# Optimization experiments

Hardware: AMD Instinct MI355X
Metric: run time of the kernel (lower is better)

## Reference

```python
import jax, jax.numpy as jnp
from jax import lax
import numpy as np

# ---- SLAYER SRM-alpha neuron / simulation constants (net_params) ----
THETA = 10.0      # spiking threshold
TAU_SR = 1.0      # PSP (synaptic response) time constant
TAU_REF = 1.0     # refractory time constant
TS = 1.0          # simulation timestep
POOL_GAIN = 1.1 * THETA  # SLAYER pool layer uses fixed weights = 1.1*theta (sum pool)

# SRM alpha kernel eps[n] = (n*Ts/tau) * exp(1 - n*Ts/tau) = c * n * d^n with
#   d = exp(-Ts/tau), c = e*Ts/tau.  Causal convolution with this kernel obeys
# a 2nd-order linear recurrence, so we implement psp as a lax.scan over time
# (the "recursive exponential temporal filter" the original does via temporal conv).

def psp(x):
    """Alpha-kernel temporal filter along last (time) axis."""
    d = float(np.exp(-TS / TAU_SR))
    c = float(np.e * TS / TAU_SR)
    xt = jnp.moveaxis(x, -1, 0)  # (T, ...)
    z = jnp.zeros_like(xt[0])
    def step(carry, u):
        p, q = carry
        q = d * (q + p)       # q[t] = sum_{n>=1} n d^n x[t-n]
        p = d * p + u         # p[t] = sum_{n>=0} d^n x[t-n]
        return (p, q), c * q
    _, y = lax.scan(step, (z, z), xt)
    return jnp.moveaxis(y, 0, -1)


def spike(u):
    """SLAYER spike generation: threshold the membrane potential at theta and
    subtract a refractory alpha kernel (-2*theta * alpha(tauRef)) from the
    future potential after each spike. Sequential scan over time."""
    d = float(np.exp(-TS / TAU_REF))
    c_r = float(-2.0 * THETA * np.e * TS / TAU_REF)
    ut = jnp.moveaxis(u, -1, 0)  # (T, ...)
    z = jnp.zeros_like(ut[0])
    def step(carry, u_t):
        p, q = carry
        q = d * (q + p)                       # refractory filter state
        s = (u_t + c_r * q >= THETA).astype(u_t.dtype)
        p = d * p + s                         # spikes feed the refractory filter
        return (p, q), s
    _, s = lax.scan(step, (z, z), ut)
    return jnp.moveaxis(s, 0, -1) / TS


def pool(x, k):
    """SLAYER pool: conv with fixed weight 1.1*theta (sum pool scaled)."""
    B, C, H, W, T = x.shape
    xr = x.reshape(B, C, H // k, k, W // k, k, T)
    return POOL_GAIN * xr.sum(axis=(3, 5))


def conv2d_t(x, W, pad):
    """Per-timestep 2D conv (SLAYER conv has time-kernel 1, no bias)."""
    B, C, H, Wd, T = x.shape
    xf = jnp.moveaxis(x, -1, 1).reshape(B * T, C, H, Wd)
    y = lax.conv_general_dilated(xf, W, (1, 1), [(pad, pad), (pad, pad)],
                                 dimension_numbers=('NCHW', 'OIHW', 'NCHW'))
    O, Ho, Wo = y.shape[1], y.shape[2], y.shape[3]
    return jnp.moveaxis(y.reshape(B, T, O, Ho, Wo), 1, -1)


def setup_inputs() -> dict:
    key = jax.random.key(0)
    ks = jax.random.split(key, 5)
    B, T = 8, 300
    s_in = jax.random.bernoulli(ks[0], 0.1, (B, 2, 128, 128, T)).astype(jnp.float32)
    # weightScale 10/50/... only affects init magnitude; choose scales that
    # produce non-degenerate spiking activity.
    W1 = jax.random.normal(ks[1], (16, 2, 5, 5), jnp.float32) * 0.5
    W2 = jax.random.normal(ks[2], (32, 16, 3, 3), jnp.float32) * 0.2
    Wf1 = jax.random.normal(ks[3], (512, 32, 8, 8), jnp.float32) * 0.05
    Wf2 = jax.random.normal(ks[4], (11, 512), jnp.float32) * 0.2
    return {"s_in": s_in, "W1": W1, "W2": W2, "Wf1": Wf1, "Wf2": Wf2}


def reference(s_in, W1, W2, Wf1, Wf2):
    s = spike(psp(pool(s_in, 4)))                 # SP0: (B,2,32,32,T)
    s = spike(psp(conv2d_t(s, W1, 2)))            # SC1: (B,16,32,32,T)
    s = spike(psp(pool(s, 2)))                    # SP1: (B,16,16,16,T)
    # SDC dropout p=0.0 -> identity
    s = spike(psp(conv2d_t(s, W2, 1)))            # SC2: (B,32,16,16,T)
    s = spike(psp(pool(s, 2)))                    # SP2: (B,32,8,8,T)
    # SDF dropout p=0.0 -> identity
    s = spike(psp(jnp.einsum('bchwt,ochw->bot', s, Wf1)))  # SF1: (B,512,T)
    s = spike(psp(jnp.einsum('bct,oc->bot', s, Wf2)))      # SF2: (B,11,T)
    return s
```

## Files before the change

### kernel.cpp

```cpp
#include <hip/hip_runtime.h>
#include <stdint.h>

#define T_STEPS 300
#define T4 75

__device__ __forceinline__ void scan_step(float x, float& pp, float& pq,
                                          float& rp, float& rq, float& s_out) {
    const float D  = 0.36787944117144233f;
    const float C  = 2.7182818284590452f;
    const float CR = -54.365636569180904f;
    const float TH = 10.0f;
    pq = D * (pq + pp);
    pp = D * pp + x;
    float u = C * pq;
    rq = D * (rq + rp);
    float s = (u + CR * rq >= TH) ? 1.0f : 0.0f;
    rp = D * rp + s;
    s_out = s;
}

#define SCAN4(v, PACK)                                                     \
    {                                                                      \
        float s0, s1, s2, s3;                                              \
        scan_step(v.x, pp, pq, rp, rq, s0);                                \
        scan_step(v.y, pp, pq, rp, rq, s1);                                \
        scan_step(v.z, pp, pq, rp, rq, s2);                                \
        scan_step(v.w, pp, pq, rp, rq, s3);                                \
        PACK = (uint32_t)s0 | ((uint32_t)s1 << 8) |                        \
               ((uint32_t)s2 << 16) | ((uint32_t)s3 << 24);                \
    }

#define FMA4(A, wc) A.x = fmaf(wc, f0, A.x); A.y = fmaf(wc, f1, A.y); \
                    A.z = fmaf(wc, f2, A.z); A.w = fmaf(wc, f3, A.w);

__global__ __launch_bounds__(256) void k_pool4(const float* __restrict__ in,
                                               float* __restrict__ z) {
    int idx = blockIdx.x * 256 + threadIdx.x;
    int t4 = idx % T4;
    int n  = idx / T4;
    int x = n & 31, y = (n >> 5) & 31, bc = n >> 10;
    const float* base = in + ((size_t)bc * 16384 + (size_t)(4 * y) * 128 + 4 * x) * T_STEPS + 4 * t4;
    float4 acc = {0.f, 0.f, 0.f, 0.f};
#pragma unroll
    for (int i = 0; i < 4; ++i)
#pragma unroll
        for (int j = 0; j < 4; ++j) {
            float4 v = *reinterpret_cast<const float4*>(base + ((size_t)i * 128 + j) * T_STEPS);
            acc.x += v.x; acc.y += v.y; acc.z += v.z; acc.w += v.w;
        }
    float4 o = {11.f * acc.x, 11.f * acc.y, 11.f * acc.z, 11.f * acc.w};
    *reinterpret_cast<float4*>(z + (size_t)n * T_STEPS + 4 * t4) = o;
}

__global__ __launch_bounds__(256) void k_scan_l0(const float* __restrict__ z,
                                                 uint32_t* __restrict__ sp, int N) {
    int n = blockIdx.x * 256 + threadIdx.x;
    if (n >= N) return;
    const float4* zp = reinterpret_cast<const float4*>(z + (size_t)n * T_STEPS);
    float pp = 0.f, pq = 0.f, rp = 0.f, rq = 0.f;
#pragma unroll 2
    for (int t4 = 0; t4 < T4; ++t4) {
        float4 v = zp[t4];
        uint32_t pack;
        SCAN4(v, pack);
        sp[(size_t)t4 * N + n] = pack;
    }
}

__global__ __launch_bounds__(256) void k_scan_plane(const float4* __restrict__ z,
                                                    uint32_t* __restrict__ sp, int N) {
    int n = blockIdx.x * 256 + threadIdx.x;
    if (n >= N) return;
    float pp = 0.f, pq = 0.f, rp = 0.f, rq = 0.f;
#pragma unroll 2
    for (int t4 = 0; t4 < T4; ++t4) {
        float4 v = z[(size_t)t4 * N + n];
        uint32_t pack;
        SCAN4(v, pack);
        sp[(size_t)t4 * N + n] = pack;
    }
}

__global__ __launch_bounds__(256) void k_scan_f32(const float* __restrict__ z,
                                                  float* __restrict__ s, int N, int ostride) {
    int n = blockIdx.x * blockDim.x + threadIdx.x;
    if (n >= N) return;
    const float4* zp = reinterpret_cast<const float4*>(z + (size_t)n * T_STEPS);
    float* spo = s + (size_t)n * ostride;
    float pp = 0.f, pq = 0.f, rp = 0.f, rq = 0.f;
    for (int it = 0; it < T4; ++it) {
        float4 v = zp[it];
        float4 o;
        scan_step(v.x, pp, pq, rp, rq, o.x);
        scan_step(v.y, pp, pq, rp, rq, o.y);
        scan_step(v.z, pp, pq, rp, rq, o.z);
        scan_step(v.w, pp, pq, rp, rq, o.w);
        *reinterpret_cast<float4*>(spo + it * 4) = o;
    }
}

template<int HW, int NIN, int NOUT>
__global__ __launch_bounds__(256) void k_pool2s(const uint32_t* __restrict__ sin,
                                                uint32_t* __restrict__ sout) {
    int n = blockIdx.x * 256 + threadIdx.x;
    if (n >= NOUT) return;
    int x = n % HW, y = (n / HW) % HW, bc = n / (HW * HW);
    const int W2d = HW * 2;
    const uint32_t* base0 = sin + (size_t)bc * W2d * W2d + (size_t)(2 * y) * W2d + 2 * x;
    float pp = 0.f, pq = 0.f, rp = 0.f, rq = 0.f;
#pragma unroll 2
    for (int t4 = 0; t4 < T4; ++t4) {
        const uint32_t* p = base0 + (size_t)t4 * NIN;
        uint32_t sum = p[0] + p[1] + p[W2d] + p[W2d + 1];
        float4 v;
        v.x = 11.f * (float)(sum & 0xffu);
        v.y = 11.f * (float)((sum >> 8) & 0xffu);
        v.z = 11.f * (float)((sum >> 16) & 0xffu);
        v.w = 11.f * (float)(sum >> 24);
        uint32_t pack;
        SCAN4(v, pack);
        sout[(size_t)t4 * NOUT + n] = pack;
    }
}

__global__ __launch_bounds__(256) void k_conv1(const uint32_t* __restrict__ s0p,
                                               const float* __restrict__ W1,
                                               float4* __restrict__ z1p) {
    __shared__ float w_lds[2][25][16];
    int bid = blockIdx.x;
    int pixblk = bid & 3;
    int t4 = (bid >> 2) % 75;
    int b  = bid / 300;
    int tid = threadIdx.x;
    for (int j = tid; j < 800; j += 256) {
        int o = j & 15, kk = (j >> 4) % 25, c = j / 400;
        w_lds[c][kk][o] = W1[(o * 2 + c) * 25 + kk];
    }
    __syncthreads();
    int pix = pixblk * 256 + tid;
    int px = pix & 31, py = pix >> 5;
    float4 acc[16];
#pragma unroll
    for (int o = 0; o < 16; ++o) acc[o] = make_float4(0.f, 0.f, 0.f, 0.f);
    const uint32_t* pb = s0p + (size_t)t4 * 16384 + (size_t)(b * 2) * 1024;
    for (int c = 0; c < 2; ++c) {
#pragma unroll
        for (int ky = 0; ky < 5; ++ky) {
            int yy = py + ky - 2;
            bool rok = (unsigned)yy < 32u;
#pragma unroll
            for (int kx = 0; kx < 5; ++kx) {
                int xx = px + kx - 2;
                uint32_t v = 0;
                if (rok && (unsigned)xx < 32u) v = pb[c * 1024 + yy * 32 + xx];
                float f0 = (float)(v & 0xffu), f1 = (float)((v >> 8) & 0xffu);
                float f2 = (float)((v >> 16) & 0xffu), f3 = (float)(v >> 24);
                int kk = ky * 5 + kx;
#pragma unroll
                for (int oo = 0; oo < 4; ++oo) {
                    float4 w4 = *reinterpret_cast<const float4*>(&w_lds[c][kk][oo * 4]);
                    FMA4(acc[oo * 4 + 0], w4.x);
                    FMA4(acc[oo * 4 + 1], w4.y);
                    FMA4(acc[oo * 4 + 2], w4.z);
                    FMA4(acc[oo * 4 + 3], w4.w);
                }
            }
        }
    }
    size_t zb = (size_t)t4 * 131072 + (size_t)(b * 16) * 1024 + pix;
#pragma unroll
    for (int o = 0; o < 16; ++o) z1p[zb + o * 1024] = acc[o];
}

__global__ __launch_bounds__(256) void k_conv2(const uint32_t* __restrict__ s2p,
                                               const float* __restrict__ W2,
                                               float4* __restrict__ z2p) {
    __shared__ float w_lds[16][9][16];
    int bid = blockIdx.x;
    int oh = bid & 1;
    int t4 = (bid >> 1) % 75;
    int b  = bid / 150;
    int tid = threadIdx.x;
    for (int j = tid; j < 2304; j += 256) {
        int o = j & 15;
        int t9 = (j >> 4) % 9;
        int c  = j / 144;
        w_lds[c][t9][o] = W2[(size_t)((oh * 16 + o) * 16 + c) * 9 + t9];
    }
    __syncthreads();
    int px = tid & 15, py = tid >> 4;
    float4 acc[16];
#pragma unroll
    for (int o = 0; o < 16; ++o) acc[o] = make_float4(0.f, 0.f, 0.f, 0.f);
    const uint32_t* pb = s2p + (size_t)t4 * 32768 + (size_t)(b * 16) * 256;
    for (int c = 0; c < 16; ++c) {
#pragma unroll
        for (int ky = 0; ky < 3; ++ky) {
            int yy = py + ky - 1;
            bool rok = (unsigned)yy < 16u;
#pragma unroll
            for (int kx = 0; kx < 3; ++kx) {
                int xx = px + kx - 1;
                uint32_t v = 0;
                if (rok && (unsigned)xx < 16u) v = pb[c * 256 + yy * 16 + xx];
                float f0 = (float)(v & 0xffu), f1 = (float)((v >> 8) & 0xffu);
                float f2 = (float)((v >> 16) & 0xffu), f3 = (float)(v >> 24);
                int t9 = ky * 3 + kx;
#pragma unroll
                for (int oo = 0; oo < 4; ++oo) {
                    float4 w4 = *reinterpret_cast<const float4*>(&w_lds[c][t9][oo * 4]);
                    FMA4(acc[oo * 4 + 0], w4.x);
                    FMA4(acc[oo * 4 + 1], w4.y);
                    FMA4(acc[oo * 4 + 2], w4.z);
                    FMA4(acc[oo * 4 + 3], w4.w);
                }
            }
        }
    }
    size_t zb = (size_t)t4 * 65536 + (size_t)(b * 32 + oh * 16) * 256 + tid;
#pragma unroll
    for (int o = 0; o < 16; ++o) z2p[zb + o * 256] = acc[o];
}

__global__ __launch_bounds__(256) void k_fc1_gemm(const uint32_t* __restrict__ s4p,
                                                  const float* __restrict__ Wf1,
                                                  float* __restrict__ z) {
    __shared__ float Wt[32][128];
    __shared__ float At[32][32];

    int tt = blockIdx.x;
    int ot = blockIdx.y;
    int b  = blockIdx.z;
    int tid = threadIdx.x;
    int othr = tid >> 3, tthr = tid & 7;
    int o0 = othr * 4;
    int t4g = tt * 8 + tthr;

    int wo = tid >> 1, wh = tid & 1;
    const float* wrow = Wf1 + (size_t)(ot * 128 + wo) * 2048 + wh * 16;
    int akk = tid & 31, at4 = tid >> 5;
    int at4g = tt * 8 + at4;
    bool aok = at4g < T4;
    const uint32_t* abase = s4p + (size_t)(aok ? at4g : 0) * 16384 + b * 2048 + akk;

    float4 acc0 = {0,0,0,0}, acc1 = {0,0,0,0}, acc2 = {0,0,0,0}, acc3 = {0,0,0,0};

    float4 wr0 = *reinterpret_cast<const float4*>(wrow + 0);
    float4 wr1 = *reinterpret_cast<const float4*>(wrow + 4);
    float4 wr2 = *reinterpret_cast<const float4*>(wrow + 8);
    float4 wr3 = *reinterpret_cast<const float4*>(wrow + 12);
    uint32_t av = aok ? abase[0] : 0u;

    for (int ks = 0; ks < 64; ++ks) {
        __syncthreads();
        int kb = wh * 16;
        Wt[kb + 0][wo] = wr0.x;  Wt[kb + 1][wo] = wr0.y;  Wt[kb + 2][wo] = wr0.z;  Wt[kb + 3][wo] = wr0.w;
        Wt[kb + 4][wo] = wr1.x;  Wt[kb + 5][wo] = wr1.y;  Wt[kb + 6][wo] = wr1.z;  Wt[kb + 7][wo] = wr1.w;
        Wt[kb + 8][wo] = wr2.x;  Wt[kb + 9][wo] = wr2.y;  Wt[kb +10][wo] = wr2.z;  Wt[kb +11][wo] = wr2.w;
        Wt[kb +12][wo] = wr3.x;  Wt[kb +13][wo] = wr3.y;  Wt[kb +14][wo] = wr3.z;  Wt[kb +15][wo] = wr3.w;
        float4 af;
        af.x = (float)(av & 0xffu);  af.y = (float)((av >> 8) & 0xffu);
        af.z = (float)((av >> 16) & 0xffu);  af.w = (float)(av >> 24);
        *reinterpret_cast<float4*>(&At[akk][at4 * 4]) = af;
        __syncthreads();
        if (ks < 63) {
            int k0 = (ks + 1) * 32;
            wr0 = *reinterpret_cast<const float4*>(wrow + k0 + 0);
            wr1 = *reinterpret_cast<const float4*>(wrow + k0 + 4);
            wr2 = *reinterpret_cast<const float4*>(wrow + k0 + 8);
            wr3 = *reinterpret_cast<const float4*>(wrow + k0 + 12);
            av = aok ? abase[k0] : 0u;
        }
#pragma unroll
        for (int kk = 0; kk < 32; ++kk) {
            float4 wv = *reinterpret_cast<const float4*>(&Wt[kk][o0]);
            float4 avv = *reinterpret_cast<const float4*>(&At[kk][tthr * 4]);
            acc0.x = fmaf(wv.x, avv.x, acc0.x); acc0.y = fmaf(wv.x, avv.y, acc0.y);
            acc0.z = fmaf(wv.x, avv.z, acc0.z); acc0.w = fmaf(wv.x, avv.w, acc0.w);
            acc1.x = fmaf(wv.y, avv.x, acc1.x); acc1.y = fmaf(wv.y, avv.y, acc1.y);
            acc1.z = fmaf(wv.y, avv.z, acc1.z); acc1.w = fmaf(wv.y, avv.w, acc1.w);
            acc2.x = fmaf(wv.z, avv.x, acc2.x); acc2.y = fmaf(wv.z, avv.y, acc2.y);
            acc2.z = fmaf(wv.z, avv.z, acc2.z); acc2.w = fmaf(wv.z, avv.w, acc2.w);
            acc3.x = fmaf(wv.w, avv.x, acc3.x); acc3.y = fmaf(wv.w, avv.y, acc3.y);
            acc3.z = fmaf(wv.w, avv.z, acc3.z); acc3.w = fmaf(wv.w, avv.w, acc3.w);
        }
    }

    if (t4g < T4) {
        size_t orow = (size_t)(b * 512 + ot * 128 + o0);
        *reinterpret_cast<float4*>(z + (orow + 0) * T_STEPS + t4g * 4) = acc0;
        *reinterpret_cast<float4*>(z + (orow + 1) * T_STEPS + t4g * 4) = acc1;
        *reinterpret_cast<float4*>(z + (orow + 2) * T_STEPS + t4g * 4) = acc2;
        *reinterpret_cast<float4*>(z + (orow + 3) * T_STEPS + t4g * 4) = acc3;
    }
}

__global__ __launch_bounds__(256) void k_fc2(const float* __restrict__ s5,
                                             const float* __restrict__ Wf2,
                                             float* __restrict__ z) {
    int idx = blockIdx.x * 256 + threadIdx.x;
    if (idx >= 6600) return;
    int t4 = idx % T4;
    int r  = idx / T4;
    int b = r & 7, o = r >> 3;
    const float* sp = s5 + (size_t)b * 512 * T_STEPS + 4 * t4;
    const float* wp = Wf2 + (size_t)o * 512;
    float a0 = 0.f, a1 = 0.f, a2 = 0.f, a3 = 0.f;
#pragma unroll 2
    for (int k = 0; k < 512; k += 4) {
        float4 wv = *reinterpret_cast<const float4*>(wp + k);
        float4 v0 = *reinterpret_cast<const float4*>(sp + (size_t)(k + 0) * T_STEPS);
        float4 v1 = *reinterpret_cast<const float4*>(sp + (size_t)(k + 1) * T_STEPS);
        float4 v2 = *reinterpret_cast<const float4*>(sp + (size_t)(k + 2) * T_STEPS);
        float4 v3 = *reinterpret_cast<const float4*>(sp + (size_t)(k + 3) * T_STEPS);
        a0 = fmaf(wv.x, v0.x, a0); a1 = fmaf(wv.x, v0.y, a1); a2 = fmaf(wv.x, v0.z, a2); a3 = fmaf(wv.x, v0.w, a3);
        a0 = fmaf(wv.y, v1.x, a0); a1 = fmaf(wv.y, v1.y, a1); a2 = fmaf(wv.y, v1.z, a2); a3 = fmaf(wv.y, v1.w, a3);
        a0 = fmaf(wv.z, v2.x, a0); a1 = fmaf(wv.z, v2.y, a1); a2 = fmaf(wv.z, v2.z, a2); a3 = fmaf(wv.z, v2.w, a3);
        a0 = fmaf(wv.w, v3.x, a0); a1 = fmaf(wv.w, v3.y, a1); a2 = fmaf(wv.w, v3.z, a2); a3 = fmaf(wv.w, v3.w, a3);
    }
    *reinterpret_cast<float4*>(z + (size_t)(b * 11 + o) * T_STEPS + 4 * t4) = make_float4(a0, a1, a2, a3);
}

__global__ void k_zero(float* out, int n) {
    int i = blockIdx.x * 256 + threadIdx.x;
    if (i < n) out[i] = 0.f;
}

extern "C" void kernel_launch(void* const* d_in, const int* in_sizes, int n_in,
                              void* d_out, int out_size, void* d_ws, size_t ws_size,
                              hipStream_t stream) {
    const float* s_in = (const float*)d_in[0];
    const float* W1   = (const float*)d_in[1];
    const float* W2   = (const float*)d_in[2];
    const float* Wf1  = (const float*)d_in[3];
    const float* Wf2  = (const float*)d_in[4];
    float* out = (float*)d_out;

    const size_t OFF_Z  = 0;
    const size_t OFF_S0 = 157286400;
    const size_t OFF_S1 = 162201600;
    const size_t OFF_S2 = 201523200;
    const size_t OFF_S3 = 211353600;
    const size_t OFF_S4 = 231014400;
    const size_t OFF_S5 = 235929600;
    const size_t NEEDED = 240844800;

    if (ws_size < NEEDED) {
        k_zero<<<(26400 + 255) / 256, 256, 0, stream>>>(out, 26400);
        return;
    }

    char* ws = (char*)d_ws;
    float*    Z   = (float*)(ws + OFF_Z);
    uint32_t* s0p = (uint32_t*)(ws + OFF_S0);
    uint32_t* s1p = (uint32_t*)(ws + OFF_S1);
    uint32_t* s2p = (uint32_t*)(ws + OFF_S2);
    uint32_t* s3p = (uint32_t*)(ws + OFF_S3);
    uint32_t* s4p = (uint32_t*)(ws + OFF_S4);
    float*    s5  = (float*)(ws + OFF_S5);

    k_pool4<<<4800, 256, 0, stream>>>(s_in, Z);
    k_scan_l0<<<64, 256, 0, stream>>>(Z, s0p, 16384);

    k_conv1<<<2400, 256, 0, stream>>>(s0p, W1, (float4*)Z);
    k_scan_plane<<<512, 256, 0, stream>>>((const float4*)Z, s1p, 131072);

    k_pool2s<16, 131072, 32768><<<128, 256, 0, stream>>>(s1p, s2p);

    k_conv2<<<1200, 256, 0, stream>>>(s2p, W2, (float4*)Z);
    k_scan_plane<<<256, 256, 0, stream>>>((const float4*)Z, s3p, 65536);

    k_pool2s<8, 65536, 16384><<<64, 256, 0, stream>>>(s3p, s4p);

    k_fc1_gemm<<<dim3(10, 4, 8), 256, 0, stream>>>(s4p, Wf1, Z);
    k_scan_f32<<<16, 256, 0, stream>>>(Z, s5, 4096, 300);

    k_fc2<<<26, 256, 0, stream>>>(s5, Wf2, Z);
    k_scan_f32<<<1, 128, 0, stream>>>(Z, out, 88, 300);
}
```

Before: 965.8 us.

## Move FC1 to bf16 MFMA with three-way split weights for fp32 accuracy

Replaces the LDS-tiled fp32 FMA GEMM for the first fully connected layer with bf16 MFMA instructions. The weights are split into high, mid and low bf16 parts on every call so the sum of three MFMAs approximates fp32 precision, and the binary spikes are exact in bf16. The pool2 spike kernel now writes bf16 spikes in a k-contiguous per-timestep layout that the MFMA operands read directly. In exchange it adds a weight-split kernel on each call, triples the weight traffic, and reads operands straight from global memory with no LDS reuse.

```diff
diff --git a/kernel.cpp b/kernel.cpp
--- a/kernel.cpp
+++ b/kernel.cpp
@@ -3,6 +3,9 @@
 
 #define T_STEPS 300
 #define T4 75
+
+typedef __attribute__((ext_vector_type(8))) short bf16x8;
+typedef __attribute__((ext_vector_type(4))) float f32x4;
 
 __device__ __forceinline__ void scan_step(float x, float& pp, float& pq,
                                           float& rp, float& rq, float& s_out) {
@@ -123,6 +126,35 @@
     }
 }
 
+__global__ __launch_bounds__(256) void k_pool2s_bf(const uint32_t* __restrict__ sin,
+                                                   ushort* __restrict__ sb) {
+    int n = blockIdx.x * 256 + threadIdx.x;
+    if (n >= 16384) return;
+    int x = n & 7, y = (n >> 3) & 7, bc = n >> 6;
+    const uint32_t* base0 = sin + (size_t)bc * 256 + (size_t)(2 * y) * 16 + 2 * x;
+    int b = n >> 11, k = n & 2047;
+    ushort* out = sb + (size_t)b * 320 * 2048 + k;
+    float pp = 0.f, pq = 0.f, rp = 0.f, rq = 0.f;
+    for (int t4 = 0; t4 < T4; ++t4) {
+        const uint32_t* p = base0 + (size_t)t4 * 65536;
+        uint32_t sum = p[0] + p[1] + p[16] + p[17];
+        float4 v;
+        v.x = 11.f * (float)(sum & 0xffu);
+        v.y = 11.f * (float)((sum >> 8) & 0xffu);
+        v.z = 11.f * (float)((sum >> 16) & 0xffu);
+        v.w = 11.f * (float)(sum >> 24);
+        float s0, s1, s2, s3;
+        scan_step(v.x, pp, pq, rp, rq, s0);
+        scan_step(v.y, pp, pq, rp, rq, s1);
+        scan_step(v.z, pp, pq, rp, rq, s2);
+        scan_step(v.w, pp, pq, rp, rq, s3);
+        out[(size_t)(t4 * 4 + 0) * 2048] = s0 != 0.f ? 0x3F80 : 0;
+        out[(size_t)(t4 * 4 + 1) * 2048] = s1 != 0.f ? 0x3F80 : 0;
+        out[(size_t)(t4 * 4 + 2) * 2048] = s2 != 0.f ? 0x3F80 : 0;
+        out[(size_t)(t4 * 4 + 3) * 2048] = s3 != 0.f ? 0x3F80 : 0;
+    }
+}
+
 __global__ __launch_bounds__(256) void k_conv1(const uint32_t* __restrict__ s0p,
                                                const float* __restrict__ W1,
                                                float4* __restrict__ z1p) {
@@ -222,76 +254,77 @@
     for (int o = 0; o < 16; ++o) z2p[zb + o * 256] = acc[o];
 }
 
-__global__ __launch_bounds__(256) void k_fc1_gemm(const uint32_t* __restrict__ s4p,
-                                                  const float* __restrict__ Wf1,
+__device__ __forceinline__ ushort f2bf(float f) {
+    uint32_t u = __float_as_uint(f);
+    u = u + 0x7fffu + ((u >> 16) & 1u);
+    return (ushort)(u >> 16);
+}
+__device__ __forceinline__ float bf2f(ushort h) {
+    return __uint_as_float((uint32_t)h << 16);
+}
+__global__ __launch_bounds__(256) void k_wsplit(const float* __restrict__ W,
+                                                ushort* __restrict__ Wh,
+                                                ushort* __restrict__ Wm,
+                                                ushort* __restrict__ Wl, int n) {
+    int i = blockIdx.x * 256 + threadIdx.x;
+    if (i >= n) return;
+    float w = W[i];
+    ushort h = f2bf(w);
+    float r1 = w - bf2f(h);
+    ushort m = f2bf(r1);
+    float r2 = r1 - bf2f(m);
+    ushort l = f2bf(r2);
+    Wh[i] = h; Wm[i] = m; Wl[i] = l;
+}
+
+__device__ __forceinline__ bf16x8 ldb(const ushort* p) {
+    return *reinterpret_cast<const bf16x8*>(p);
+}
+__global__ __launch_bounds__(256) void k_fc1_mfma(const ushort* __restrict__ Wh,
+                                                  const ushort* __restrict__ Wm,
+                                                  const ushort* __restrict__ Wl,
+                                                  const ushort* __restrict__ sb,
                                                   float* __restrict__ z) {
-    __shared__ float Wt[32][128];
-    __shared__ float At[32][32];
-
-    int tt = blockIdx.x;
-    int ot = blockIdx.y;
+    int tid = threadIdx.x, lane = tid & 63, wv = tid >> 6;
+    int l15 = lane & 15, l4 = lane >> 4;
+    int oA = blockIdx.x * 64 + (wv & 1) * 32 + l15;
+    int t  = blockIdx.y * 32 + (wv >> 1) * 16 + l15;
     int b  = blockIdx.z;
-    int tid = threadIdx.x;
-    int othr = tid >> 3, tthr = tid & 7;
-    int o0 = othr * 4;
-    int t4g = tt * 8 + tthr;
-
-    int wo = tid >> 1, wh = tid & 1;
-    const float* wrow = Wf1 + (size_t)(ot * 128 + wo) * 2048 + wh * 16;
-    int akk = tid & 31, at4 = tid >> 5;
-    int at4g = tt * 8 + at4;
-    bool aok = at4g < T4;
-    const uint32_t* abase = s4p + (size_t)(aok ? at4g : 0) * 16384 + b * 2048 + akk;
-
-    float4 acc0 = {0,0,0,0}, acc1 = {0,0,0,0}, acc2 = {0,0,0,0}, acc3 = {0,0,0,0};
-
-    float4 wr0 = *reinterpret_cast<const float4*>(wrow + 0);
-    float4 wr1 = *reinterpret_cast<const float4*>(wrow + 4);
-    float4 wr2 = *reinterpret_cast<const float4*>(wrow + 8);
-    float4 wr3 = *reinterpret_cast<const float4*>(wrow + 12);
-    uint32_t av = aok ? abase[0] : 0u;
+    size_t a0 = (size_t)oA * 2048 + l4 * 8;
+    size_t a1 = a0 + 16 * 2048;
+    size_t bo = ((size_t)b * 320 + t) * 2048 + l4 * 8;
+
+    f32x4 acc0 = {0.f, 0.f, 0.f, 0.f};
+    f32x4 acc1 = {0.f, 0.f, 0.f, 0.f};
+
+    bf16x8 h0 = ldb(Wh + a0), h1 = ldb(Wh + a1);
+    bf16x8 m0 = ldb(Wm + a0), m1 = ldb(Wm + a1);
+    bf16x8 l0 = ldb(Wl + a0), l1 = ldb(Wl + a1);
+    bf16x8 bb = ldb(sb + bo);
 
     for (int ks = 0; ks < 64; ++ks) {
-        __syncthreads();
-        int kb = wh * 16;
-        Wt[kb + 0][wo] = wr0.x;  Wt[kb + 1][wo] = wr0.y;  Wt[kb + 2][wo] = wr0.z;  Wt[kb + 3][wo] = wr0.w;
-        Wt[kb + 4][wo] = wr1.x;  Wt[kb + 5][wo] = wr1.y;  Wt[kb + 6][wo] = wr1.z;  Wt[kb + 7][wo] = wr1.w;
-        Wt[kb + 8][wo] = wr2.x;  Wt[kb + 9][wo] = wr2.y;  Wt[kb +10][wo] = wr2.z;  Wt[kb +11][wo] = wr2.w;
-        Wt[kb +12][wo] = wr3.x;  Wt[kb +13][wo] = wr3.y;  Wt[kb +14][wo] = wr3.z;  Wt[kb +15][wo] = wr3.w;
-        float4 af;
-        af.x = (float)(av & 0xffu);  af.y = (float)((av >> 8) & 0xffu);
-        af.z = (float)((av >> 16) & 0xffu);  af.w = (float)(av >> 24);
-        *reinterpret_cast<float4*>(&At[akk][at4 * 4]) = af;
-        __syncthreads();
-        if (ks < 63) {
-            int k0 = (ks + 1) * 32;
-            wr0 = *reinterpret_cast<const float4*>(wrow + k0 + 0);
-            wr1 = *reinterpret_cast<const float4*>(wrow + k0 + 4);
-            wr2 = *reinterpret_cast<const float4*>(wrow + k0 + 8);
-            wr3 = *reinterpret_cast<const float4*>(wrow + k0 + 12);
-            av = aok ? abase[k0] : 0u;
-        }
-#pragma unroll
-        for (int kk = 0; kk < 32; ++kk) {
-            float4 wv = *reinterpret_cast<const float4*>(&Wt[kk][o0]);
-            float4 avv = *reinterpret_cast<const float4*>(&At[kk][tthr * 4]);
-            acc0.x = fmaf(wv.x, avv.x, acc0.x); acc0.y = fmaf(wv.x, avv.y, acc0.y);
-            acc0.z = fmaf(wv.x, avv.z, acc0.z); acc0.w = fmaf(wv.x, avv.w, acc0.w);
-            acc1.x = fmaf(wv.y, avv.x, acc1.x); acc1.y = fmaf(wv.y, avv.y, acc1.y);
-            acc1.z = fmaf(wv.y, avv.z, acc1.z); acc1.w = fmaf(wv.y, avv.w, acc1.w);
-            acc2.x = fmaf(wv.z, avv.x, acc2.x); acc2.y = fmaf(wv.z, avv.y, acc2.y);
-            acc2.z = fmaf(wv.z, avv.z, acc2.z); acc2.w = fmaf(wv.z, avv.w, acc2.w);
-            acc3.x = fmaf(wv.w, avv.x, acc3.x); acc3.y = fmaf(wv.w, avv.y, acc3.y);
-            acc3.z = fmaf(wv.w, avv.z, acc3.z); acc3.w = fmaf(wv.w, avv.w, acc3.w);
-        }
-    }
-
-    if (t4g < T4) {
-        size_t orow = (size_t)(b * 512 + ot * 128 + o0);
-        *reinterpret_cast<float4*>(z + (orow + 0) * T_STEPS + t4g * 4) = acc0;
-        *reinterpret_cast<float4*>(z + (orow + 1) * T_STEPS + t4g * 4) = acc1;
-        *reinterpret_cast<float4*>(z + (orow + 2) * T_STEPS + t4g * 4) = acc2;
-        *reinterpret_cast<float4*>(z + (orow + 3) * T_STEPS + t4g * 4) = acc3;
+        int kn = (ks < 63) ? (ks + 1) * 32 : 0;
+        bf16x8 nh0 = ldb(Wh + a0 + kn), nh1 = ldb(Wh + a1 + kn);
+        bf16x8 nm0 = ldb(Wm + a0 + kn), nm1 = ldb(Wm + a1 + kn);
+        bf16x8 nl0 = ldb(Wl + a0 + kn), nl1 = ldb(Wl + a1 + kn);
+        bf16x8 nbb = ldb(sb + bo + kn);
+        acc0 = __builtin_amdgcn_mfma_f32_16x16x32_bf16(h0, bb, acc0, 0, 0, 0);
+        acc1 = __builtin_amdgcn_mfma_f32_16x16x32_bf16(h1, bb, acc1, 0, 0, 0);
+        acc0 = __builtin_amdgcn_mfma_f32_16x16x32_bf16(m0, bb, acc0, 0, 0, 0);
+        acc1 = __builtin_amdgcn_mfma_f32_16x16x32_bf16(m1, bb, acc1, 0, 0, 0);
+        acc0 = __builtin_amdgcn_mfma_f32_16x16x32_bf16(l0, bb, acc0, 0, 0, 0);
+        acc1 = __builtin_amdgcn_mfma_f32_16x16x32_bf16(l1, bb, acc1, 0, 0, 0);
+        h0 = nh0; h1 = nh1; m0 = nm0; m1 = nm1; l0 = nl0; l1 = nl1; bb = nbb;
+    }
+
+    if (t < T_STEPS) {
+        int orow = blockIdx.x * 64 + (wv & 1) * 32 + l4 * 4;
+        float* zr = z + ((size_t)b * 512 + orow) * T_STEPS + t;
+        zr[0 * T_STEPS] = acc0.x;  zr[1 * T_STEPS] = acc0.y;
+        zr[2 * T_STEPS] = acc0.z;  zr[3 * T_STEPS] = acc0.w;
+        float* zr2 = zr + 16 * T_STEPS;
+        zr2[0 * T_STEPS] = acc1.x; zr2[1 * T_STEPS] = acc1.y;
+        zr2[2 * T_STEPS] = acc1.z; zr2[3 * T_STEPS] = acc1.w;
     }
 }
 
@@ -341,9 +374,12 @@
     const size_t OFF_S1 = 162201600;
     const size_t OFF_S2 = 201523200;
     const size_t OFF_S3 = 211353600;
-    const size_t OFF_S4 = 231014400;
-    const size_t OFF_S5 = 235929600;
-    const size_t NEEDED = 240844800;
+    const size_t OFF_SB = 231014400;
+    const size_t OFF_S5 = 241500160;
+    const size_t OFF_WH = 246415360;
+    const size_t OFF_WM = 248512512;
+    const size_t OFF_WL = 250609664;
+    const size_t NEEDED = 252706816;
 
     if (ws_size < NEEDED) {
         k_zero<<<(26400 + 255) / 256, 256, 0, stream>>>(out, 26400);
@@ -356,8 +392,13 @@
     uint32_t* s1p = (uint32_t*)(ws + OFF_S1);
     uint32_t* s2p = (uint32_t*)(ws + OFF_S2);
     uint32_t* s3p = (uint32_t*)(ws + OFF_S3);
-    uint32_t* s4p = (uint32_t*)(ws + OFF_S4);
+    ushort*   sbf = (ushort*)(ws + OFF_SB);
     float*    s5  = (float*)(ws + OFF_S5);
+    ushort*   Wh  = (ushort*)(ws + OFF_WH);
+    ushort*   Wm  = (ushort*)(ws + OFF_WM);
+    ushort*   Wl  = (ushort*)(ws + OFF_WL);
+
+    k_wsplit<<<4096, 256, 0, stream>>>(Wf1, Wh, Wm, Wl, 512 * 2048);
 
     k_pool4<<<4800, 256, 0, stream>>>(s_in, Z);
     k_scan_l0<<<64, 256, 0, stream>>>(Z, s0p, 16384);
@@ -370,9 +411,9 @@
     k_conv2<<<1200, 256, 0, stream>>>(s2p, W2, (float4*)Z);
     k_scan_plane<<<256, 256, 0, stream>>>((const float4*)Z, s3p, 65536);
 
-    k_pool2s<8, 65536, 16384><<<64, 256, 0, stream>>>(s3p, s4p);
-
-    k_fc1_gemm<<<dim3(10, 4, 8), 256, 0, stream>>>(s4p, Wf1, Z);
+    k_pool2s_bf<<<64, 256, 0, stream>>>(s3p, sbf);
+
+    k_fc1_mfma<<<dim3(8, 10, 8), 256, 0, stream>>>(Wh, Wm, Wl, sbf, Z);
     k_scan_f32<<<16, 256, 0, stream>>>(Z, s5, 4096, 300);
 
     k_fc2<<<26, 256, 0, stream>>>(s5, Wf2, Z);
```

Result: slower. 989.6 us (+2.5%).
